# Optimization experiments

Measured on AMD Instinct MI355X. Metric: run time of the kernel, lower is better.

## Reference

```python
import jax, jax.numpy as jnp
import numpy as np


def _banded_diag_mean(a, b, r):
    """For each (batch i, row j) return mean of (a[i] @ b[i].T)[j, j-r:j+r+1],
    computed without materializing the LxL matrix. Windows are clipped to
    [max(0,j-r), min(L, j+r+1)].  a, b: [B, L, D]."""
    B, L, _ = a.shape
    sums = jnp.zeros((B, L), a.dtype)
    counts = jnp.zeros((L,), a.dtype)
    for d in range(-r, r + 1):  # small fixed set of 2r+1 diagonals
        if d >= 0:
            dots = jnp.einsum('bld,bld->bl', a[:, :L - d], b[:, d:])
            sums = sums.at[:, :L - d].add(dots)
            counts = counts.at[:L - d].add(1.0)
        else:
            dots = jnp.einsum('bld,bld->bl', a[:, -d:], b[:, :L + d])
            sums = sums.at[:, -d:].add(dots)
            counts = counts.at[-d:].add(1.0)
    return sums / counts


def setup_inputs() -> dict:
    key = jax.random.key(0)
    k1, k2, k3 = jax.random.split(key, 3)
    B, L, D_in, D_feat = 8, 1024, 512, 256
    return {
        'feature1': jax.random.normal(k1, (B, L, D_in), jnp.float32),
        'feature2': jax.random.normal(k2, (B, L, D_in), jnp.float32),
        'W': jax.random.normal(k3, (D_in, D_feat), jnp.float32) / np.sqrt(D_in),
        'b': jnp.zeros((D_feat,), jnp.float32),
        'positive_range_self': 4,
        'positive_range_tgt': 4,
    }


def reference(feature1, feature2, W, b, positive_range_self, positive_range_tgt):
    # MLPLayer projection (shared eval_func for both inputs): linear + relu
    emb_1 = jax.nn.relu(feature1 @ W + b)  # [B, L, Df]
    emb_2 = jax.nn.relu(feature2 @ W + b)  # [B, L, Df]
    B, L, Df = emb_1.shape
    N = B * L

    positive = jnp.einsum('bld,bld->bl', emb_1, emb_2)  # [B, L]
    if positive_range_self > 0:
        positive = positive + _banded_diag_mean(emb_1, emb_1, positive_range_self)
        positive = positive + _banded_diag_mean(emb_2, emb_2, positive_range_self)
    if positive_range_tgt > 0:
        positive = positive + _banded_diag_mean(emb_1, emb_2, positive_range_tgt)
    positive = positive.reshape(N)

    e1 = emb_1.reshape(N, Df)
    e2 = emb_2.reshape(N, Df)
    sim_matrix = e1 @ e2.T  # [N, N]
    negative = jax.nn.logsumexp(sim_matrix, axis=-1) - jnp.log(jnp.asarray(N, sim_matrix.dtype))

    nce_loss = jnp.mean(-positive + negative)
    return nce_loss
```

## Files before the change

### kernel.cpp

```cpp
#include <hip/hip_runtime.h>
#include <hip/hip_bf16.h>
#include <math.h>

#define DIN 512
#define DF 256
#define LSEQ 1024
#define NTOT 8192

typedef __attribute__((ext_vector_type(8))) short short8;
typedef __attribute__((ext_vector_type(4))) short short4v;
typedef __attribute__((ext_vector_type(4))) float f32x4;

__device__ __forceinline__ short f2bf(float x) {
  union { float f; unsigned u; } un; un.f = x;
  unsigned r = un.u + 0x7fffu + ((un.u >> 16) & 1u);
  return (short)(r >> 16);
}
__device__ __forceinline__ float bf2f(short s) {
  union { unsigned u; float f; } un; un.u = ((unsigned)(unsigned short)s) << 16;
  return un.f;
}

typedef __attribute__((address_space(1))) const unsigned char AS1c;
typedef __attribute__((address_space(3))) unsigned char AS3;
__device__ __forceinline__ void gload16(const void* g, void* l) {
  __builtin_amdgcn_global_load_lds((AS1c*)g, (AS3*)l, 16, 0, 0);
}
#define CFENCE() asm volatile("" ::: "memory")
#define EXP2R(x) __builtin_amdgcn_exp2f(x)
#define L2E 1.44269504089f
#define THRL 11.5416f
#define LN2 0.69314718056f

__global__ __launch_bounds__(256) void prep_w_kernel(const float* __restrict__ W,
                                                     short* __restrict__ Wt) {
  __shared__ short t[64 * 70];
  const int tid = threadIdx.x;
  const int k0 = (blockIdx.x & 7) * 64;
  const int c0 = (blockIdx.x >> 3) * 64;
  const int cl = tid & 63, kq = tid >> 6;
#pragma unroll
  for (int r = 0; r < 16; ++r) {
    int kl = kq * 16 + r;
    t[cl * 70 + kl] = f2bf(W[(size_t)(k0 + kl) * DF + c0 + cl]);
  }
  __syncthreads();
  const int kl2 = tid & 63, cq = tid >> 6;
#pragma unroll
  for (int r = 0; r < 16; ++r) {
    int cl2 = cq * 16 + r;
    Wt[(size_t)(c0 + cl2) * DIN + k0 + kl2] = t[cl2 * 70 + kl2];
  }
}

#define PBM 64
#define PBK 64
#define PROW 72

__global__ __launch_bounds__(256) void proj_kernel(const float* __restrict__ f1,
                                                   const float* __restrict__ f2,
                                                   const short* __restrict__ Wt,
                                                   const float* __restrict__ bias,
                                                   short* __restrict__ emb1,
                                                   short* __restrict__ emb2) {
  const float* feat = blockIdx.y ? f2 : f1;
  short* emb = blockIdx.y ? emb2 : emb1;
  __shared__ short ldsA[PBM * PROW];
  __shared__ short ldsB[DF * PROW];
  const int tid = threadIdx.x;
  const int lane = tid & 63, wv = tid >> 6;
  const int wrow = (wv & 1) * 32, wcol = (wv >> 1) * 128;
  const int l15 = lane & 15, lk = (lane >> 4) * 8;
  const int rowbase = blockIdx.x * PBM;

  f32x4 acc[2][8];
#pragma unroll
  for (int mi = 0; mi < 2; ++mi)
#pragma unroll
    for (int nf = 0; nf < 8; ++nf) acc[mi][nf] = f32x4{0.f, 0.f, 0.f, 0.f};

  for (int kb = 0; kb < DIN; kb += PBK) {
    __syncthreads();
#pragma unroll
    for (int i = 0; i < 4; ++i) {
      int flat = tid * 4 + i;
      int r = flat >> 4, kq = (flat & 15) * 4;
      f32x4 v = *(const f32x4*)(feat + (size_t)(rowbase + r) * DIN + kb + kq);
      short4v h;
      h[0] = f2bf(v[0]); h[1] = f2bf(v[1]); h[2] = f2bf(v[2]); h[3] = f2bf(v[3]);
      *(short4v*)(ldsA + r * PROW + kq) = h;
    }
#pragma unroll
    for (int i = 0; i < 8; ++i) {
      int c = tid, kq = i * 8;
      short8 v = *(const short8*)(Wt + (size_t)c * DIN + kb + kq);
      *(short8*)(ldsB + c * PROW + kq) = v;
    }
    __syncthreads();
#pragma unroll
    for (int kk = 0; kk < 2; ++kk) {
      short8 af[2], bf[8];
#pragma unroll
      for (int mi = 0; mi < 2; ++mi)
        af[mi] = *(const short8*)(ldsA + (wrow + mi * 16 + l15) * PROW + kk * 32 + lk);
#pragma unroll
      for (int nf = 0; nf < 8; ++nf)
        bf[nf] = *(const short8*)(ldsB + (wcol + nf * 16 + l15) * PROW + kk * 32 + lk);
#pragma unroll
      for (int mi = 0; mi < 2; ++mi)
#pragma unroll
        for (int nf = 0; nf < 8; ++nf)
          acc[mi][nf] = __builtin_amdgcn_mfma_f32_16x16x32_bf16(af[mi], bf[nf], acc[mi][nf], 0, 0, 0);
    }
  }
  const int r4 = (lane >> 4) * 4;
#pragma unroll
  for (int mi = 0; mi < 2; ++mi) {
    int row0 = rowbase + wrow + mi * 16 + r4;
#pragma unroll
    for (int nf = 0; nf < 8; ++nf) {
      int col = wcol + nf * 16 + l15;
      float bb = bias[col];
#pragma unroll
      for (int r = 0; r < 4; ++r) {
        float v = acc[mi][nf][r] + bb;
        v = v > 0.f ? v : 0.f;
        emb[(size_t)(row0 + r) * DF + col] = f2bf(v);
      }
    }
  }
}

#define POSR 32
#define PSTR 258

__global__ __launch_bounds__(256) void positive_kernel(const short* __restrict__ emb1,
                                                       const short* __restrict__ emb2,
                                                       const int* __restrict__ prs,
                                                       const int* __restrict__ prt,
                                                       float* __restrict__ pos) {
  __shared__ short s1[40 * PSTR];
  __shared__ short s2[40 * PSTR];
  const int tid = threadIdx.x;
  const int b = blockIdx.x >> 5;
  const int j0 = (blockIdx.x & 31) * POSR;
  const int rs = prs[0], rt = prt[0];

  {
    const int rr = tid >> 6, c4 = (tid & 63) * 4;
#pragma unroll
    for (int it = 0; it < 10; ++it) {
      int r = it * 4 + rr;
      int g = j0 - 4 + r;
      short4v v1 = short4v{0, 0, 0, 0}, v2 = short4v{0, 0, 0, 0};
      if (g >= 0 && g < LSEQ) {
        size_t off = (size_t)(b * LSEQ + g) * DF + c4;
        v1 = *(const short4v*)(emb1 + off);
        v2 = *(const short4v*)(emb2 + off);
      }
      *(short4v*)(s1 + r * PSTR + c4) = v1;
      *(short4v*)(s2 + r * PSTR + c4) = v2;
    }
  }
  __syncthreads();

  const int lane = tid & 63, wv = tid >> 6;
  for (int q = 0; q < 8; ++q) {
    const int j = j0 + wv * 8 + q;
    const int rl = wv * 8 + q + 4;
    float a1[4], a2[4];
    {
      short4v v1 = *(const short4v*)(s1 + rl * PSTR + lane * 4);
      short4v v2 = *(const short4v*)(s2 + rl * PSTR + lane * 4);
#pragma unroll
      for (int i = 0; i < 4; ++i) { a1[i] = bf2f(v1[i]); a2[i] = bf2f(v2[i]); }
    }
    float dot12 = 0.f, p11 = 0.f, p22 = 0.f, p12 = 0.f;
#pragma unroll
    for (int i = 0; i < 4; ++i) dot12 += a1[i] * a2[i];
    int rmax = rs > rt ? rs : rt;
    for (int d = -rmax; d <= rmax; ++d) {
      int k = j + d;
      if (k < 0 || k >= LSEQ) continue;
      int kl = rl + d;
      short4v w1 = *(const short4v*)(s1 + kl * PSTR + lane * 4);
      short4v w2 = *(const short4v*)(s2 + kl * PSTR + lane * 4);
      float d11 = 0.f, d22 = 0.f, d12 = 0.f;
#pragma unroll
      for (int i = 0; i < 4; ++i) {
        float e1k = bf2f(w1[i]), e2k = bf2f(w2[i]);
        d11 += a1[i] * e1k;
        d22 += a2[i] * e2k;
        d12 += a1[i] * e2k;
      }
      if (d >= -rs && d <= rs) { p11 += d11; p22 += d22; }
      if (d >= -rt && d <= rt) { p12 += d12; }
    }
#pragma unroll
    for (int m = 1; m < 64; m <<= 1) {
      dot12 += __shfl_xor(dot12, m);
      p11 += __shfl_xor(p11, m);
      p22 += __shfl_xor(p22, m);
      p12 += __shfl_xor(p12, m);
    }
    if (lane == 0) {
      float res = dot12;
      if (rs > 0) {
        int lo = j - rs < 0 ? 0 : j - rs;
        int hi = j + rs > LSEQ - 1 ? LSEQ - 1 : j + rs;
        res += (p11 + p22) / (float)(hi - lo + 1);
      }
      if (rt > 0) {
        int lo = j - rt < 0 ? 0 : j - rt;
        int hi = j + rt > LSEQ - 1 ? LSEQ - 1 : j + rt;
        res += p12 / (float)(hi - lo + 1);
      }
      pos[b * LSEQ + j] = res;
    }
  }
}

#define NBM 128
#define NBN 32
#define NCHUNK 16
#define CHW (NTOT / NCHUNK)
#define NT (CHW / NBN)

__global__ __launch_bounds__(256, 3) void negative_kernel(const short* __restrict__ e1,
                                                          const short* __restrict__ e2,
                                                          float* __restrict__ mpart,
                                                          float* __restrict__ spart) {
  __shared__ short ldsB[2][NBN * DF];
  const int tid = threadIdx.x;
  const int lane = tid & 63, wv = tid >> 6;
  const int l15 = lane & 15, lk16 = lane >> 4;
  const int rowbase = blockIdx.x * NBM + wv * 32;
  const short* colbase = e2 + (size_t)(blockIdx.y * CHW) * DF;

  const int src_off = (tid & 31) * DF + (tid >> 5) * 8;
  const int dst_off = wv * 512;

  auto stage = [&](int tt) {
    const short* nb = colbase + (size_t)tt * NBN * DF + src_off;
    short* db = (short*)ldsB[tt & 1] + dst_off;
#pragma unroll
    for (int i = 0; i < 4; ++i)
      gload16(nb + i * 64, db + i * 2048);
  };

  stage(0);
  CFENCE();
  short8 a[2][8];
#pragma unroll
  for (int mi = 0; mi < 2; ++mi)
#pragma unroll
    for (int ks = 0; ks < 8; ++ks)
      a[mi][ks] = *(const short8*)(e1 + (size_t)(rowbase + mi * 16 + l15) * DF + ks * 32 + lk16 * 8);
  CFENCE();
  stage(1);
  CFENCE();

  float mrunL[8], srun[8];
#pragma unroll
  for (int i = 0; i < 8; ++i) { mrunL[i] = 0.f; srun[i] = 0.f; }

  for (int t = 0; t < NT; ++t) {
    if (t < NT - 1) asm volatile("s_waitcnt vmcnt(4)" ::: "memory");
    else            asm volatile("s_waitcnt vmcnt(0)" ::: "memory");
    __builtin_amdgcn_s_barrier();
    const short* bbase = (const short*)ldsB[t & 1] + lk16 * 256 + l15 * 8;

    f32x4 acc[2][2];
#pragma unroll
    for (int mi = 0; mi < 2; ++mi)
#pragma unroll
      for (int nf = 0; nf < 2; ++nf) acc[mi][nf] = f32x4{0.f, 0.f, 0.f, 0.f};

    __builtin_amdgcn_s_setprio(1);
#pragma unroll
    for (int ks = 0; ks < 8; ++ks) {
      short8 b0 = *(const short8*)(bbase + ks * 1024);
      short8 b1 = *(const short8*)(bbase + ks * 1024 + 128);
#pragma unroll
      for (int mi = 0; mi < 2; ++mi) {
        acc[mi][0] = __builtin_amdgcn_mfma_f32_16x16x32_bf16(a[mi][ks], b0, acc[mi][0], 0, 0, 0);
        acc[mi][1] = __builtin_amdgcn_mfma_f32_16x16x32_bf16(a[mi][ks], b1, acc[mi][1], 0, 0, 0);
      }
    }
    __builtin_amdgcn_s_setprio(0);

    float g0[8], g1[8], m01[8];
#pragma unroll
    for (int s = 0; s < 8; ++s) {
      float v0 = acc[s >> 2][0][s & 3], v1 = acc[s >> 2][1][s & 3];
      g0[s] = __builtin_fmaf(v0, L2E, -mrunL[s]);
      g1[s] = __builtin_fmaf(v1, L2E, -mrunL[s]);
      m01[s] = fmaxf(g0[s], g1[s]);
    }
    float x0 = fmaxf(fmaxf(m01[0], m01[1]), fmaxf(m01[2], m01[3]));
    float x1 = fmaxf(fmaxf(m01[4], m01[5]), fmaxf(m01[6], m01[7]));
    if (__builtin_expect(__any(fmaxf(x0, x1) > THRL), 0)) {
#pragma unroll
      for (int s = 0; s < 8; ++s) {
        float dL = fmaxf(m01[s], 0.f);
        srun[s] = srun[s] * EXP2R(-dL) + EXP2R(g0[s] - dL) + EXP2R(g1[s] - dL);
        mrunL[s] += dL;
      }
    } else {
#pragma unroll
      for (int s = 0; s < 8; ++s)
        srun[s] += EXP2R(g0[s]) + EXP2R(g1[s]);
    }
    __builtin_amdgcn_s_barrier();
    CFENCE();
    if (t + 2 < NT) stage(t + 2);
  }

#pragma unroll
  for (int s = 0; s < 8; ++s) {
    float m = mrunL[s], sv = srun[s];
#pragma unroll
    for (int msk = 1; msk < 16; msk <<= 1) {
      float mo = __shfl_xor(m, msk);
      float so = __shfl_xor(sv, msk);
      float mn = fmaxf(m, mo);
      sv = sv * EXP2R(m - mn) + so * EXP2R(mo - mn);
      m = mn;
    }
    if (l15 == 0) {
      int row = rowbase + (s >> 2) * 16 + lk16 * 4 + (s & 3);
      mpart[blockIdx.y * NTOT + row] = m;
      spart[blockIdx.y * NTOT + row] = sv;
    }
  }
}

__global__ __launch_bounds__(256) void finalize1_kernel(const float* __restrict__ pos,
                                                        const float* __restrict__ mpart,
                                                        const float* __restrict__ spart,
                                                        float* __restrict__ partial) {
  __shared__ float red[4];
  int row = blockIdx.x * 256 + threadIdx.x;
  float m = -1e30f;
#pragma unroll
  for (int c = 0; c < NCHUNK; ++c) m = fmaxf(m, mpart[c * NTOT + row]);
  float s = 0.f;
#pragma unroll
  for (int c = 0; c < NCHUNK; ++c) s += spart[c * NTOT + row] * EXP2R(mpart[c * NTOT + row] - m);
  float v = (m + __builtin_amdgcn_logf(s)) * LN2 - pos[row];
#pragma unroll
  for (int msk = 1; msk < 64; msk <<= 1) v += __shfl_xor(v, msk);
  if ((threadIdx.x & 63) == 0) red[threadIdx.x >> 6] = v;
  __syncthreads();
  if (threadIdx.x == 0) partial[blockIdx.x] = red[0] + red[1] + red[2] + red[3];
}

__global__ __launch_bounds__(64) void finalize2_kernel(const float* __restrict__ partial,
                                                       float* __restrict__ out) {
  int lane = threadIdx.x;
  float v = lane < 32 ? partial[lane] : 0.f;
#pragma unroll
  for (int msk = 1; msk < 64; msk <<= 1) v += __shfl_xor(v, msk);
  if (lane == 0) out[0] = v / (float)NTOT - logf((float)NTOT);
}

extern "C" void kernel_launch(void* const* d_in, const int* in_sizes, int n_in,
                              void* d_out, int out_size, void* d_ws, size_t ws_size,
                              hipStream_t stream) {
  const float* f1 = (const float*)d_in[0];
  const float* f2 = (const float*)d_in[1];
  const float* W = (const float*)d_in[2];
  const float* bias = (const float*)d_in[3];
  const int* prs = (const int*)d_in[4];
  const int* prt = (const int*)d_in[5];
  float* out = (float*)d_out;

  char* ws = (char*)d_ws;
  short* Wt = (short*)(ws);
  short* emb1 = (short*)(ws + 262144);
  short* emb2 = (short*)(ws + 262144 + 4194304);
  float* pos = (float*)(ws + 8650752);
  float* mpart = (float*)(ws + 8683520);
  float* spart = (float*)(ws + 9207808);
  float* partial = (float*)(ws + 9732096);

  prep_w_kernel<<<32, 256, 0, stream>>>(W, Wt);
  proj_kernel<<<dim3(NTOT / PBM, 2), 256, 0, stream>>>(f1, f2, Wt, bias, emb1, emb2);
  positive_kernel<<<NTOT / POSR, 256, 0, stream>>>(emb1, emb2, prs, prt, pos);
  negative_kernel<<<dim3(NTOT / NBM, NCHUNK), 256, 0, stream>>>(emb1, emb2, mpart, spart);
  finalize1_kernel<<<32, 256, 0, stream>>>(pos, mpart, spart, partial);
  finalize2_kernel<<<1, 64, 0, stream>>>(partial, out);
}
```

Measured before the change: 96.60 us.

## Use k-block LDS layout with direct global-to-LDS loads; simplify online logsumexp

The projection kernel now stores A and W tiles in a k-block-major LDS layout with no padding and loads the W tile with global_load_lds instead of going through registers. The similarity kernel's lazy-rescaling logsumexp, with its threshold check and base-2 running max, is replaced by a plain per-step online max/rescale using __expf, and finalize is adjusted to match. The LDS change targets load overhead in the projection GEMM. The online-softmax change adds exp work and a max on every tile, which likely costs time in the dominant similarity loop.

```diff
diff --git a/kernel.cpp b/kernel.cpp
--- a/kernel.cpp
+++ b/kernel.cpp
@@ -27,9 +27,6 @@
   __builtin_amdgcn_global_load_lds((AS1c*)g, (AS3*)l, 16, 0, 0);
 }
 #define CFENCE() asm volatile("" ::: "memory")
-#define EXP2R(x) __builtin_amdgcn_exp2f(x)
-#define L2E 1.44269504089f
-#define THRL 11.5416f
 #define LN2 0.69314718056f
 
 __global__ __launch_bounds__(256) void prep_w_kernel(const float* __restrict__ W,
@@ -55,7 +52,6 @@
 
 #define PBM 64
 #define PBK 64
-#define PROW 72
 
 __global__ __launch_bounds__(256) void proj_kernel(const float* __restrict__ f1,
                                                    const float* __restrict__ f2,
@@ -65,12 +61,12 @@
                                                    short* __restrict__ emb2) {
   const float* feat = blockIdx.y ? f2 : f1;
   short* emb = blockIdx.y ? emb2 : emb1;
-  __shared__ short ldsA[PBM * PROW];
-  __shared__ short ldsB[DF * PROW];
+  __shared__ short ldsA[8 * 64 * 8];
+  __shared__ short ldsB[8 * 256 * 8];
   const int tid = threadIdx.x;
   const int lane = tid & 63, wv = tid >> 6;
   const int wrow = (wv & 1) * 32, wcol = (wv >> 1) * 128;
-  const int l15 = lane & 15, lk = (lane >> 4) * 8;
+  const int l15 = lane & 15, lk16 = lane >> 4;
   const int rowbase = blockIdx.x * PBM;
 
   f32x4 acc[2][8];
@@ -79,33 +75,34 @@
 #pragma unroll
     for (int nf = 0; nf < 8; ++nf) acc[mi][nf] = f32x4{0.f, 0.f, 0.f, 0.f};
 
-  for (int kb = 0; kb < DIN; kb += PBK) {
+  for (int K0 = 0; K0 < DIN; K0 += PBK) {
     __syncthreads();
 #pragma unroll
-    for (int i = 0; i < 4; ++i) {
-      int flat = tid * 4 + i;
-      int r = flat >> 4, kq = (flat & 15) * 4;
-      f32x4 v = *(const f32x4*)(feat + (size_t)(rowbase + r) * DIN + kb + kq);
-      short4v h;
-      h[0] = f2bf(v[0]); h[1] = f2bf(v[1]); h[2] = f2bf(v[2]); h[3] = f2bf(v[3]);
-      *(short4v*)(ldsA + r * PROW + kq) = h;
-    }
-#pragma unroll
-    for (int i = 0; i < 8; ++i) {
-      int c = tid, kq = i * 8;
-      short8 v = *(const short8*)(Wt + (size_t)c * DIN + kb + kq);
-      *(short8*)(ldsB + c * PROW + kq) = v;
+    for (int i = 0; i < 8; ++i)
+      gload16(Wt + (size_t)tid * DIN + K0 + i * 8, ldsB + (i * 256 + tid) * 8);
+#pragma unroll
+    for (int i = 0; i < 2; ++i) {
+      int g = i * 256 + tid;
+      int kb = g >> 6, r = g & 63;
+      const float* src = feat + (size_t)(rowbase + r) * DIN + K0 + kb * 8;
+      f32x4 v0 = *(const f32x4*)(src);
+      f32x4 v1 = *(const f32x4*)(src + 4);
+      short8 h;
+      h[0] = f2bf(v0[0]); h[1] = f2bf(v0[1]); h[2] = f2bf(v0[2]); h[3] = f2bf(v0[3]);
+      h[4] = f2bf(v1[0]); h[5] = f2bf(v1[1]); h[6] = f2bf(v1[2]); h[7] = f2bf(v1[3]);
+      *(short8*)(ldsA + g * 8) = h;
     }
     __syncthreads();
 #pragma unroll
     for (int kk = 0; kk < 2; ++kk) {
+      const int kb = kk * 4 + lk16;
       short8 af[2], bf[8];
 #pragma unroll
       for (int mi = 0; mi < 2; ++mi)
-        af[mi] = *(const short8*)(ldsA + (wrow + mi * 16 + l15) * PROW + kk * 32 + lk);
+        af[mi] = *(const short8*)(ldsA + (kb * 64 + wrow + mi * 16 + l15) * 8);
 #pragma unroll
       for (int nf = 0; nf < 8; ++nf)
-        bf[nf] = *(const short8*)(ldsB + (wcol + nf * 16 + l15) * PROW + kk * 32 + lk);
+        bf[nf] = *(const short8*)(ldsB + (kb * 256 + wcol + nf * 16 + l15) * 8);
 #pragma unroll
       for (int mi = 0; mi < 2; ++mi)
 #pragma unroll
@@ -260,9 +257,9 @@
   stage(1);
   CFENCE();
 
-  float mrunL[8], srun[8];
-#pragma unroll
-  for (int i = 0; i < 8; ++i) { mrunL[i] = 0.f; srun[i] = 0.f; }
+  float mrun[8], srun[8];
+#pragma unroll
+  for (int i = 0; i < 8; ++i) { mrun[i] = -1e30f; srun[i] = 0.f; }
 
   for (int t = 0; t < NT; ++t) {
     if (t < NT - 1) asm volatile("s_waitcnt vmcnt(4)" ::: "memory");
@@ -289,50 +286,42 @@
     }
     __builtin_amdgcn_s_setprio(0);
 
-    float g0[8], g1[8], m01[8];
-#pragma unroll
-    for (int s = 0; s < 8; ++s) {
-      float v0 = acc[s >> 2][0][s & 3], v1 = acc[s >> 2][1][s & 3];
-      g0[s] = __builtin_fmaf(v0, L2E, -mrunL[s]);
-      g1[s] = __builtin_fmaf(v1, L2E, -mrunL[s]);
-      m01[s] = fmaxf(g0[s], g1[s]);
-    }
-    float x0 = fmaxf(fmaxf(m01[0], m01[1]), fmaxf(m01[2], m01[3]));
-    float x1 = fmaxf(fmaxf(m01[4], m01[5]), fmaxf(m01[6], m01[7]));
-    if (__builtin_expect(__any(fmaxf(x0, x1) > THRL), 0)) {
-#pragma unroll
-      for (int s = 0; s < 8; ++s) {
-        float dL = fmaxf(m01[s], 0.f);
-        srun[s] = srun[s] * EXP2R(-dL) + EXP2R(g0[s] - dL) + EXP2R(g1[s] - dL);
-        mrunL[s] += dL;
-      }
-    } else {
-#pragma unroll
-      for (int s = 0; s < 8; ++s)
-        srun[s] += EXP2R(g0[s]) + EXP2R(g1[s]);
-    }
+#pragma unroll
+    for (int mi = 0; mi < 2; ++mi)
+#pragma unroll
+      for (int r = 0; r < 4; ++r) {
+        int s8 = mi * 4 + r;
+        float v0 = acc[mi][0][r], v1 = acc[mi][1][r];
+        float mo = mrun[s8];
+        float mn = fmaxf(mo, fmaxf(v0, v1));
+        mrun[s8] = mn;
+        srun[s8] = srun[s8] * __expf(mo - mn) + __expf(v0 - mn) + __expf(v1 - mn);
+      }
     __builtin_amdgcn_s_barrier();
     CFENCE();
     if (t + 2 < NT) stage(t + 2);
   }
 
 #pragma unroll
-  for (int s = 0; s < 8; ++s) {
-    float m = mrunL[s], sv = srun[s];
-#pragma unroll
-    for (int msk = 1; msk < 16; msk <<= 1) {
-      float mo = __shfl_xor(m, msk);
-      float so = __shfl_xor(sv, msk);
-      float mn = fmaxf(m, mo);
-      sv = sv * EXP2R(m - mn) + so * EXP2R(mo - mn);
-      m = mn;
-    }
-    if (l15 == 0) {
-      int row = rowbase + (s >> 2) * 16 + lk16 * 4 + (s & 3);
-      mpart[blockIdx.y * NTOT + row] = m;
-      spart[blockIdx.y * NTOT + row] = sv;
-    }
-  }
+  for (int mi = 0; mi < 2; ++mi)
+#pragma unroll
+    for (int r = 0; r < 4; ++r) {
+      int s8 = mi * 4 + r;
+      float m = mrun[s8], s = srun[s8];
+#pragma unroll
+      for (int msk = 1; msk < 16; msk <<= 1) {
+        float mo = __shfl_xor(m, msk);
+        float so = __shfl_xor(s, msk);
+        float mn = fmaxf(m, mo);
+        s = s * __expf(m - mn) + so * __expf(mo - mn);
+        m = mn;
+      }
+      if (l15 == 0) {
+        int row = rowbase + mi * 16 + lk16 * 4 + r;
+        mpart[blockIdx.y * NTOT + row] = m;
+        spart[blockIdx.y * NTOT + row] = s;
+      }
+    }
 }
 
 __global__ __launch_bounds__(256) void finalize1_kernel(const float* __restrict__ pos,
@@ -346,8 +335,8 @@
   for (int c = 0; c < NCHUNK; ++c) m = fmaxf(m, mpart[c * NTOT + row]);
   float s = 0.f;
 #pragma unroll
-  for (int c = 0; c < NCHUNK; ++c) s += spart[c * NTOT + row] * EXP2R(mpart[c * NTOT + row] - m);
-  float v = (m + __builtin_amdgcn_logf(s)) * LN2 - pos[row];
+  for (int c = 0; c < NCHUNK; ++c) s += spart[c * NTOT + row] * __expf(mpart[c * NTOT + row] - m);
+  float v = m + LN2 * __builtin_amdgcn_logf(s) - pos[row];
 #pragma unroll
   for (int msk = 1; msk < 64; msk <<= 1) v += __shfl_xor(v, msk);
   if ((threadIdx.x & 63) == 0) red[threadIdx.x >> 6] = v;
```

After: 96.70 us. Within noise of the previous version (+0.1%).
